# Kernel optimization log

Hardware: AMD Instinct MI355X
Metric: run time of the kernel (lower is better)

Reference implementation:

```python
import jax, jax.numpy as jnp
import numpy as np

B, C1, H, W = 2, 128, 64, 64
C_ = C1 // 2


def _conv2d(x, w, b, pad, dil):
    out = jax.lax.conv_general_dilated(
        x, w, (1, 1), [(pad, pad), (pad, pad)], rhs_dilation=(dil, dil),
        dimension_numbers=('NCHW', 'OIHW', 'NCHW'))
    return out + b[None, :, None, None]


def _deform_dw(x, off_w, off_b, w, k, pad, dil):
    # Depthwise DeformConv2d (v1, no modulation), offset_groups=1, stride=1.
    Bn, C, Hn, Wn = x.shape
    K = k * k
    offsets = _conv2d(x, off_w, off_b, pad, dil)          # [B, 2K, H, W]
    off = offsets.reshape(Bn, K, 2, Hn, Wn)               # (dy, dx) per kernel pt
    ky = jnp.repeat(jnp.arange(k) * dil, k).astype(x.dtype)   # [K]
    kx = jnp.tile(jnp.arange(k) * dil, k).astype(x.dtype)     # [K]
    py = off[:, :, 0] + (jnp.arange(Hn, dtype=x.dtype)[:, None] - pad) + ky[None, :, None, None]
    px = off[:, :, 1] + (jnp.arange(Wn, dtype=x.dtype)[None, :] - pad) + kx[None, :, None, None]
    y0 = jnp.floor(py); x0 = jnp.floor(px)
    ly = py - y0; lx = px - x0
    y0i = y0.astype(jnp.int32); x0i = x0.astype(jnp.int32)
    xf = x.reshape(Bn, C, Hn * Wn)

    def corner(yi, xi, wgt):
        valid = (yi >= 0) & (yi < Hn) & (xi >= 0) & (xi < Wn)
        idx = (jnp.clip(yi, 0, Hn - 1) * Wn + jnp.clip(xi, 0, Wn - 1)).reshape(Bn, -1)
        v = jax.vmap(lambda xb, ib: xb[:, ib])(xf, idx).reshape(Bn, C, K, Hn, Wn)
        return v * (wgt * valid.astype(x.dtype))[:, None]

    val = (corner(y0i, x0i, (1 - ly) * (1 - lx))
           + corner(y0i, x0i + 1, (1 - ly) * lx)
           + corner(y0i + 1, x0i, ly * (1 - lx))
           + corner(y0i + 1, x0i + 1, ly * lx))      # [B, C, K, H, W]
    return jnp.einsum('bckhw,ck->bchw', val, w.reshape(C, K))


def _forward(x, cv0_off_w, cv0_off_b, cv0_w, cvs_off_w, cvs_off_b, cvs_w,
             c0_off_w, c0_off_b, c0_w, cs_off_w, cs_off_b, cs_w,
             conv1_w, conv1_b, conv2_w, conv2_b):
    c = x.shape[1] // 2
    y0, y1 = x[:, :c], x[:, c:]
    a0 = _deform_dw(y0, cv0_off_w, cv0_off_b, cv0_w, 3, 1, 1)
    a0 = _deform_dw(a0, cvs_off_w, cvs_off_b, cvs_w, 5, 6, 3)
    a0 = _conv2d(a0, conv1_w, conv1_b, 0, 1)
    a1 = _deform_dw(y1, c0_off_w, c0_off_b, c0_w, 5, 2, 1)
    a1 = _deform_dw(a1, cs_off_w, cs_off_b, cs_w, 7, 9, 3)
    a1 = _conv2d(a1, conv2_w, conv2_b, 0, 1)
    return x * jnp.concatenate([a0, a1], axis=1)


def setup_inputs() -> dict:
    key = jax.random.key(0)
    ks = jax.random.split(key, 18)
    n = lambda k, sh, s: jax.random.normal(k, sh, dtype=jnp.float32) * s
    return {
        'x': n(ks[0], (B, C1, H, W), 1.0),
        'cv0_off_w': n(ks[1], (18, C_, 3, 3), 0.05),  'cv0_off_b': n(ks[2], (18,), 0.05),
        'cv0_w': n(ks[3], (C_, 1, 3, 3), 0.1),
        'cvs_off_w': n(ks[4], (50, C_, 5, 5), 0.05),  'cvs_off_b': n(ks[5], (50,), 0.05),
        'cvs_w': n(ks[6], (C_, 1, 5, 5), 0.1),
        'c0_off_w': n(ks[7], (50, C_, 5, 5), 0.05),   'c0_off_b': n(ks[8], (50,), 0.05),
        'c0_w': n(ks[9], (C_, 1, 5, 5), 0.1),
        'cs_off_w': n(ks[10], (98, C_, 7, 7), 0.05),  'cs_off_b': n(ks[11], (98,), 0.05),
        'cs_w': n(ks[12], (C_, 1, 7, 7), 0.1),
        'conv1_w': n(ks[13], (C_, C_, 1, 1), 0.1),    'conv1_b': n(ks[14], (C_,), 0.05),
        'conv2_w': n(ks[15], (C_, C_, 1, 1), 0.1),    'conv2_b': n(ks[16], (C_,), 0.05),
    }


def reference(x, cv0_off_w, cv0_off_b, cv0_w, cvs_off_w, cvs_off_b, cvs_w,
              c0_off_w, c0_off_b, c0_w, cs_off_w, cs_off_b, cs_w,
              conv1_w, conv1_b, conv2_w, conv2_b):
    return _forward(x, cv0_off_w, cv0_off_b, cv0_w, cvs_off_w, cvs_off_b, cvs_w,
                    c0_off_w, c0_off_b, c0_w, cs_off_w, cs_off_b, cs_w,
                    conv1_w, conv1_b, conv2_w, conv2_b)
```

## Files before the change

kernel.cpp:

```cpp
#include <hip/hip_runtime.h>
#include <hip/hip_bf16.h>

#define HW   4096

typedef __bf16 bf_t;
typedef __bf16 bf8_t __attribute__((ext_vector_type(8)));
typedef __bf16 bf2_t __attribute__((ext_vector_type(2)));
typedef __bf16 bf4v_t __attribute__((ext_vector_type(4)));
typedef float  f4_t  __attribute__((ext_vector_type(4)));
typedef float  f2_t  __attribute__((ext_vector_type(2)));
typedef int    i4_t  __attribute__((ext_vector_type(4)));

#define OFF_A    0
#define OFF_B    409600
#define A1_F32   1212416
#define B1_F32   1736704
#define A2_F32   2260992
#define B2_F32   2785280
#define XA_F32   3309568
#define XB_F32   3833856
#define XA_HI    4358144
#define XA_LO    4620288
#define XB_HI    4882432
#define XB_LO    5144576
#define A1_HI    5406720
#define A1_LO    5668864
#define B1_HI    5931008
#define B1_LO    6193152
#define AW_A1    6455296
#define AW_B1    6464512
#define AW_A2    6515712
#define AW_B2    6566912
#define DW_A1    6767616
#define DW_B1    6768192
#define DW_A2    6769792
#define DW_B2    6771392
#define WS_TOT   6774528

__device__ __align__(16) float g_ws[WS_TOT];

__device__ __forceinline__ bf8_t bf8_zero() {
    bf8_t v;
#pragma unroll
    for (int j = 0; j < 8; ++j) v[j] = (bf_t)0.f;
    return v;
}

__device__ __forceinline__ void prep_wA_dev(const float* wg, int aw_off,
                                            int Cout, int K, int NCOT, int lb) {
    const int KK = K * K;
    const int total = KK * NCOT * 128;
    const int idx = lb * 256 + threadIdx.x;
    if (idx >= total) return;
    bf_t* aw = (bf_t*)(g_ws + aw_off);
    int lane = idx & 63;
    int kh   = (idx >> 6) & 1;
    int cot  = (idx >> 7) % NCOT;
    int tap  = idx / (128 * NCOT);
    int co   = cot * 16 + (lane & 15);
    int ci0  = kh * 32 + (lane >> 4) * 8;
    bf8_t v;
#pragma unroll
    for (int j = 0; j < 8; ++j) {
        float f = (co < Cout) ? wg[(co * 64 + ci0 + j) * KK + tap] : 0.f;
        v[j] = (bf_t)f;
    }
    *(bf8_t*)&aw[(long)idx * 8] = v;
}

__device__ __forceinline__ void prep_dwT_dev(const float* w, int dst_off,
                                             int KK, int lb) {
    const int idx = lb * 256 + threadIdx.x;
    if (idx < KK * 64) {
        int c = idx & 63, kk = idx >> 6;
        g_ws[dst_off + kk * 64 + c] = w[c * KK + kk];
    }
}

__global__ __launch_bounds__(256) void prep_split_kernel(
    const float* __restrict__ x,
    const float* cv0_off_w, const float* c0_off_w,
    const float* cvs_off_w, const float* cs_off_w,
    const float* cv0_w, const float* c0_w,
    const float* cvs_w, const float* cs_w)
{
    __shared__ float lds[16 * 68];
    const int bi = blockIdx.x;
    if (bi < 335) {
        if      (bi < 9)   prep_wA_dev(cv0_off_w, AW_A1, 18, 3, 2, bi);
        else if (bi < 59)  prep_wA_dev(c0_off_w,  AW_B1, 50, 5, 4, bi - 9);
        else if (bi < 109) prep_wA_dev(cvs_off_w, AW_A2, 50, 5, 4, bi - 59);
        else if (bi < 305) prep_wA_dev(cs_off_w,  AW_B2, 98, 7, 8, bi - 109);
        else if (bi < 308) prep_dwT_dev(cv0_w, DW_A1, 9,  bi - 305);
        else if (bi < 315) prep_dwT_dev(c0_w,  DW_B1, 25, bi - 308);
        else if (bi < 322) prep_dwT_dev(cvs_w, DW_A2, 25, bi - 315);
        else               prep_dwT_dev(cs_w,  DW_B2, 49, bi - 322);
        return;
    }
    const int s  = bi - 335;
    const int b  = s & 1;
    const int br = (s >> 1) & 1;
    const int p0 = (s >> 2) * 16;
    const float* sb = x + (long)b * (128 * HW) + (long)br * (64 * HW);
    bf_t*  dhi = (bf_t*)(g_ws + (br ? XB_HI : XA_HI));
    bf_t*  dlo = (bf_t*)(g_ws + (br ? XB_LO : XA_LO));
    float* df  = g_ws + (br ? XB_F32 : XA_F32);
    const int t = threadIdx.x;
    {
        const int px = t & 15;
        const int c0 = t >> 4;
#pragma unroll
        for (int pass = 0; pass < 4; ++pass) {
            int ci = c0 + pass * 16;
            lds[px * 68 + ci] = sb[ci * HW + p0 + px];
        }
    }
    __syncthreads();
    if (t < 128) {
        int px = t >> 3, q = t & 7;
        bf8_t vh, vl;
        f4_t  f0, f1;
#pragma unroll
        for (int j = 0; j < 8; ++j) {
            float a = lds[px * 68 + q * 8 + j];
            bf_t hcast = (bf_t)a;
            vh[j] = hcast;
            vl[j] = (bf_t)(a - (float)hcast);
            if (j < 4) f0[j] = a; else f1[j - 4] = a;
        }
        long base = (((long)b * 4096 + p0 + px) * 64) + q * 8;
        *(bf8_t*)&dhi[base] = vh;
        *(bf8_t*)&dlo[base] = vl;
        *(f4_t*)&df[base]     = f0;
        *(f4_t*)&df[base + 4] = f1;
    }
}

template<int K, int DIL, int PAD, int NCOT, int CPG>
__device__ __forceinline__ void mfma_conv_dev(
    int bx, int by, bf_t* smem,
    int hi_off, int lo_off, int aw_off, const float* __restrict__ bias,
    int dst_off, int Cout)
{
    constexpr int COLS = 64 + 2 * PAD;
    const bf_t* shi = (const bf_t*)(g_ws + hi_off);
    const bf_t* slo = (const bf_t*)(g_ws + lo_off);
    const bf_t* aw  = (const bf_t*)(g_ws + aw_off);
    float* dst = g_ws + dst_off;
    bf_t* lds0 = smem;
    bf_t* lds1 = smem + COLS * 72;

    const int t    = threadIdx.x;
    const int lane = t & 63;
    const int wv   = t >> 6;
    const int b    = bx >> 6;
    const int h    = bx & 63;
    const int ct0  = by * CPG;

    const int n0 = lane & 15;
    const int kq = lane >> 4;

    f4_t acc[CPG];
#pragma unroll
    for (int i = 0; i < CPG; ++i) acc[i] = (f4_t){0.f, 0.f, 0.f, 0.f};

    for (int ky = 0; ky < K; ++ky) {
        const int ih = h - PAD + ky * DIL;
        __syncthreads();
        if ((unsigned)ih < 64u) {
            const long rowb = ((long)b * 4096 + ih * 64) * 64;
            for (int c = t; c < COLS * 8; c += 256) {
                int col = c >> 3, q = c & 7;
                int iw = col - PAD;
                bf8_t vh, vl;
                if ((unsigned)iw < 64u) {
                    vh = *(const bf8_t*)&shi[rowb + iw * 64 + q * 8];
                    vl = *(const bf8_t*)&slo[rowb + iw * 64 + q * 8];
                } else { vh = bf8_zero(); vl = bf8_zero(); }
                *(bf8_t*)&lds0[col * 72 + q * 8] = vh;
                *(bf8_t*)&lds1[col * 72 + q * 8] = vl;
            }
        } else {
            bf8_t z = bf8_zero();
            for (int c = t; c < COLS * 8; c += 256) {
                int col = c >> 3, q = c & 7;
                *(bf8_t*)&lds0[col * 72 + q * 8] = z;
                *(bf8_t*)&lds1[col * 72 + q * 8] = z;
            }
        }
        __syncthreads();
#pragma unroll
        for (int kx = 0; kx < K; ++kx) {
            const int tap = ky * K + kx;
            bf8_t afr[CPG][2];
#pragma unroll
            for (int ct = 0; ct < CPG; ++ct)
#pragma unroll
                for (int kh = 0; kh < 2; ++kh)
                    afr[ct][kh] = *(const bf8_t*)
                        &aw[((((long)tap * NCOT + ct0 + ct) * 2 + kh) * 64 + lane) * 8];
            const int colb = (wv * 16 + n0 + kx * DIL) * 72;
#pragma unroll
            for (int kh = 0; kh < 2; ++kh) {
                const bf8_t bh = *(const bf8_t*)&lds0[colb + kh * 32 + kq * 8];
                const bf8_t bl = *(const bf8_t*)&lds1[colb + kh * 32 + kq * 8];
#pragma unroll
                for (int ct = 0; ct < CPG; ++ct) {
                    acc[ct] = __builtin_amdgcn_mfma_f32_16x16x32_bf16(
                        afr[ct][kh], bh, acc[ct], 0, 0, 0);
                    acc[ct] = __builtin_amdgcn_mfma_f32_16x16x32_bf16(
                        afr[ct][kh], bl, acc[ct], 0, 0, 0);
                }
            }
        }
    }

    const int w = wv * 16 + n0;
#pragma unroll
    for (int ct = 0; ct < CPG; ++ct) {
#pragma unroll
        for (int r = 0; r < 4; ++r) {
            int co = (ct0 + ct) * 16 + kq * 4 + r;
            if (co < Cout)
                dst[((long)b * Cout + co) * HW + h * 64 + w] = acc[ct][r] + bias[co];
        }
    }
}

__global__ __launch_bounds__(256) void conv_s1_kernel(
    const float* __restrict__ biasA, const float* __restrict__ biasB)
{
    extern __shared__ __align__(16) bf_t smem1[];
    const int bi = blockIdx.x;
    const int g = bi / 3, r = bi % 3;
    if (r == 0)
        mfma_conv_dev<3, 1, 1, 2, 2>(g & 127, 0, smem1,
                                     XA_HI, XA_LO, AW_A1, biasA, OFF_A, 18);
    else {
        const int s = 2 * g + (r - 1);
        mfma_conv_dev<5, 1, 2, 4, 2>(s & 127, s >> 7, smem1,
                                     XB_HI, XB_LO, AW_B1, biasB, OFF_B, 50);
    }
}

__global__ __launch_bounds__(256) void conv_s2_kernel(
    const float* __restrict__ biasA, const float* __restrict__ biasB)
{
    extern __shared__ __align__(16) bf_t smem2[];
    const int bi = blockIdx.x;
    const int s = bi >> 1;
    if ((bi & 1) == 0)
        mfma_conv_dev<5, 3, 6, 4, 2>(s & 127, s >> 7, smem2,
                                     A1_HI, A1_LO, AW_A2, biasA, OFF_A, 50);
    else
        mfma_conv_dev<7, 3, 9, 8, 4>(s & 127, s >> 7, smem2,
                                     B1_HI, B1_LO, AW_B2, biasB, OFF_B, 98);
}

template<int KK, int WRITE_HILO>
__device__ __forceinline__ void sample_fused_dev(
    int bx, float* recs, float* dwl, int src_off, int off_off, int dwt_off,
    int dst_off, int hi_off, int lo_off, int K, int pad, int dil)
{
    const int t   = threadIdx.x;
    const int pgi = ((bx & 7) << 7) | (bx >> 3);

    for (int rec = t; rec < 8 * KK; rec += 256) {
        const int pxl = rec & 7;
        const int kk  = rec >> 3;
        const int pg  = pgi * 8 + pxl;
        const int b   = pg >> 12;
        const int p   = pg & 4095;
        const int h   = p >> 6, w = p & 63;
        const float oy = g_ws[off_off + ((long)(b * 2 * KK + 2 * kk)) * HW + p];
        const float ox = g_ws[off_off + ((long)(b * 2 * KK + 2 * kk + 1)) * HW + p];
        const float py = oy + (float)(h - pad + (kk / K) * dil);
        const float px = ox + (float)(w - pad + (kk % K) * dil);
        const float fy = floorf(py), fx = floorf(px);
        const float ly = py - fy,    lx = px - fx;
        const int y0 = (int)fy, x0 = (int)fx;
        const int y1 = y0 + 1,  x1 = x0 + 1;
        const float ry0 = ((unsigned)y0 < 64u) ? (1.f - ly) : 0.f;
        const float ry1 = ((unsigned)y1 < 64u) ? ly : 0.f;
        const float cx0 = ((unsigned)x0 < 64u) ? (1.f - lx) : 0.f;
        const float cx1 = ((unsigned)x1 < 64u) ? lx : 0.f;
        const int xbase = min(max(x0, 0), 62);
        const float sA = (xbase == x0) ? cx0 : ((xbase == x1) ? cx1 : 0.f);
        const float sB = ((xbase + 1) == x1) ? cx1
                                             : (((xbase + 1) == x0) ? cx0 : 0.f);
        const int y0c = min(max(y0, 0), 63), y1c = min(max(y1, 0), 63);
        const int a0 = (y0c * 64 + xbase) * 256;
        const int a1 = (y1c * 64 + xbase) * 256;
        float* rp = &recs[rec * 8];
        f4_t r0, r1;
        r0[0] = ry0 * sA; r0[1] = ry0 * sB;
        r0[2] = __int_as_float(a0); r0[3] = 0.f;
        r1[0] = ry1 * sA; r1[1] = ry1 * sB;
        r1[2] = __int_as_float(a1); r1[3] = 0.f;
        *(f4_t*)rp       = r0;
        *(f4_t*)(rp + 4) = r1;
    }

    for (int e = t; e < KK * 64; e += 256) dwl[e] = g_ws[dwt_off + e];
    __syncthreads();

    const int lane = t & 63;
    const int half = (lane >> 5) & 1;
    const int sub  = (lane >> 4) & 1;
    const int q    = lane & 15;
    const int wv   = t >> 6;
    const int px0  = wv * 2, px1 = wv * 2 + 1;
    const int pg0  = pgi * 8 + px0;
    const int b    = pg0 >> 12;

    const char*  sbl = (const char*)(g_ws + src_off + ((long)b << 18))
                       + sub * 256 + q * 16;
    const float* dwp = dwl + q * 4;

    f4_t acc0 = {0.f, 0.f, 0.f, 0.f};
    f4_t acc1 = {0.f, 0.f, 0.f, 0.f};
#pragma unroll
    for (int kk = 0; kk < KK; ++kk) {
        const f4_t r0 = *(const f4_t*)&recs[(kk * 8 + px0) * 8 + half * 4];
        const f4_t r1 = *(const f4_t*)&recs[(kk * 8 + px1) * 8 + half * 4];
        const f4_t dw = *(const f4_t*)(dwp + kk * 64);
        const float w0 = sub ? r0[1] : r0[0];
        const float w1 = sub ? r1[1] : r1[0];
        const f4_t v0 = *(const f4_t*)(sbl + __float_as_int(r0[2]));
        const f4_t v1 = *(const f4_t*)(sbl + __float_as_int(r1[2]));
#pragma unroll
        for (int c = 0; c < 4; ++c) {
            acc0[c] = fmaf(dw[c] * w0, v0[c], acc0[c]);
            acc1[c] = fmaf(dw[c] * w1, v1[c], acc1[c]);
        }
    }

#pragma unroll
    for (int c = 0; c < 4; ++c) {
        acc0[c] += __shfl_xor(acc0[c], 16);
        acc0[c] += __shfl_xor(acc0[c], 32);
        acc1[c] += __shfl_xor(acc1[c], 16);
        acc1[c] += __shfl_xor(acc1[c], 32);
    }

    const int p0 = pg0 & 4095;
    const long ob0 = ((long)b * 4096 + p0) * 64 + q * 4;
    const long ob1 = ob0 + 64;
    const int grp = lane >> 4;
    if (WRITE_HILO) {
        if (grp == 0) {
            *(f4_t*)&g_ws[dst_off + ob0] = acc0;
        } else if (grp == 1) {
            *(f4_t*)&g_ws[dst_off + ob1] = acc1;
        } else if (grp == 2) {
            bf4v_t h0, l0;
#pragma unroll
            for (int c = 0; c < 4; ++c) {
                bf_t hh = (bf_t)acc0[c];
                h0[c] = hh; l0[c] = (bf_t)(acc0[c] - (float)hh);
            }
            *(bf4v_t*)&((bf_t*)(g_ws + hi_off))[ob0] = h0;
            *(bf4v_t*)&((bf_t*)(g_ws + lo_off))[ob0] = l0;
        } else {
            bf4v_t h1, l1;
#pragma unroll
            for (int c = 0; c < 4; ++c) {
                bf_t hh = (bf_t)acc1[c];
                h1[c] = hh; l1[c] = (bf_t)(acc1[c] - (float)hh);
            }
            *(bf4v_t*)&((bf_t*)(g_ws + hi_off))[ob1] = h1;
            *(bf4v_t*)&((bf_t*)(g_ws + lo_off))[ob1] = l1;
        }
    } else {
        if (grp == 0)      *(f4_t*)&g_ws[dst_off + ob0] = acc0;
        else if (grp == 1) *(f4_t*)&g_ws[dst_off + ob1] = acc1;
    }
}

template<int KA, int KB, int WRITE_HILO>
__global__ __launch_bounds__(256) void sample_kernel(
    int srcA, int offA, int dwtA, int dstA, int hiA, int loA, int padA, int dilA,
    int srcB, int offB, int dwtB, int dstB, int hiB, int loB, int padB, int dilB)
{
    constexpr int KKmax = KB * KB;
    __shared__ __align__(16) float recs[8 * KKmax * 8];
    __shared__ __align__(16) float dwl[KKmax * 64];
    const int bx = blockIdx.x;
    const int s = bx >> 1;
    if ((bx & 1) == 0)
        sample_fused_dev<KA * KA, WRITE_HILO>(s, recs, dwl, srcA, offA, dwtA,
                                              dstA, hiA, loA, KA, padA, dilA);
    else
        sample_fused_dev<KB * KB, WRITE_HILO>(s, recs, dwl, srcB, offB, dwtB,
                                              dstB, hiB, loB, KB, padB, dilB);
}

__global__ __launch_bounds__(256) void final_kernel(
    const float* __restrict__ x,
    int aA_off, int aB_off,
    const float* __restrict__ w1, const float* __restrict__ b1,
    const float* __restrict__ w2, const float* __restrict__ b2,
    float* __restrict__ out)
{
    __shared__ float atile[64 * 65];
    __shared__ float wlds[64 * 32];
    const int t  = threadIdx.x;
    const int p0 = blockIdx.x * 64;
    const int by = blockIdx.y;
    const int b  = blockIdx.z;
    const bool brB  = (by >> 1) != 0;
    const int  cbase = (by & 1) * 32;
    const float* a  = g_ws + (brB ? aB_off : aA_off) + (long)b * (4096 * 64);
    const float* wg = brB ? w2 : w1;
    const float* bg = brB ? b2 : b1;

    {
        const int ci = t & 63;
        const int pxg = (t >> 6) * 16;
#pragma unroll
        for (int i = 0; i < 16; ++i) {
            int px = pxg + i;
            atile[px * 65 + ci] = a[(long)(p0 + px) * 64 + ci];
        }
    }
    for (int e = t; e < 2048; e += 256) {
        int col = e & 31, ci = e >> 5;
        wlds[ci * 32 + col] = wg[(cbase + col) * 64 + ci];
    }
    __syncthreads();

    const int px  = t & 63;
    const int cog = t >> 6;
    float acc[8] = {0, 0, 0, 0, 0, 0, 0, 0};
    for (int ci = 0; ci < 64; ++ci) {
        const float av = atile[px * 65 + ci];
        const float* wr = &wlds[ci * 32 + cog * 8];
#pragma unroll
        for (int j = 0; j < 8; ++j) acc[j] = fmaf(av, wr[j], acc[j]);
    }

    const int p = p0 + px;
#pragma unroll
    for (int j = 0; j < 8; ++j) {
        const int co = cbase + cog * 8 + j;
        const int cg = (brB ? 64 : 0) + co;
        const long o = ((long)b * 128 + cg) * HW + p;
        out[o] = (acc[j] + bg[co]) * x[o];
    }
}

extern "C" void kernel_launch(void* const* d_in, const int* in_sizes, int n_in,
                              void* d_out, int out_size, void* d_ws, size_t ws_size,
                              hipStream_t stream) {
    const float* x         = (const float*)d_in[0];
    const float* cv0_off_w = (const float*)d_in[1];
    const float* cv0_off_b = (const float*)d_in[2];
    const float* cv0_w     = (const float*)d_in[3];
    const float* cvs_off_w = (const float*)d_in[4];
    const float* cvs_off_b = (const float*)d_in[5];
    const float* cvs_w     = (const float*)d_in[6];
    const float* c0_off_w  = (const float*)d_in[7];
    const float* c0_off_b  = (const float*)d_in[8];
    const float* c0_w      = (const float*)d_in[9];
    const float* cs_off_w  = (const float*)d_in[10];
    const float* cs_off_b  = (const float*)d_in[11];
    const float* cs_w      = (const float*)d_in[12];
    const float* conv1_w   = (const float*)d_in[13];
    const float* conv1_b   = (const float*)d_in[14];
    const float* conv2_w   = (const float*)d_in[15];
    const float* conv2_b   = (const float*)d_in[16];
    float* out = (float*)d_out;
    (void)d_ws; (void)ws_size;

    prep_split_kernel<<<dim3(1359), 256, 0, stream>>>(
        x, cv0_off_w, c0_off_w, cvs_off_w, cs_off_w, cv0_w, c0_w, cvs_w, cs_w);

    conv_s1_kernel<<<dim3(384), 256, 19584, stream>>>(cv0_off_b, c0_off_b);

    sample_kernel<3, 5, 1><<<dim3(2048), 256, 0, stream>>>(
        XA_F32, OFF_A, DW_A1, A1_F32, A1_HI, A1_LO, 1, 1,
        XB_F32, OFF_B, DW_B1, B1_F32, B1_HI, B1_LO, 2, 1);

    conv_s2_kernel<<<dim3(512), 256, 23616, stream>>>(cvs_off_b, cs_off_b);

    sample_kernel<5, 7, 0><<<dim3(2048), 256, 0, stream>>>(
        A1_F32, OFF_A, DW_A2, A2_F32, 0, 0, 6, 3,
        B1_F32, OFF_B, DW_B2, B2_F32, 0, 0, 9, 3);

    final_kernel<<<dim3(64, 4, 2), 256, 0, stream>>>(
        x, A2_F32, B2_F32, conv1_w, conv1_b, conv2_w, conv2_b, out);
}
```

Measured before the change: 204.7 us.

## Fuse all six stages into one cooperative persistent kernel with grid syncs

```diff
diff --git a/kernel.cpp b/kernel.cpp
--- a/kernel.cpp
+++ b/kernel.cpp
@@ -1,15 +1,16 @@
 #include <hip/hip_runtime.h>
 #include <hip/hip_bf16.h>
+#include <hip/hip_cooperative_groups.h>
+
+namespace cg = cooperative_groups;
 
 #define HW   4096
+#define NBLK 768
 
 typedef __bf16 bf_t;
 typedef __bf16 bf8_t __attribute__((ext_vector_type(8)));
-typedef __bf16 bf2_t __attribute__((ext_vector_type(2)));
 typedef __bf16 bf4v_t __attribute__((ext_vector_type(4)));
 typedef float  f4_t  __attribute__((ext_vector_type(4)));
-typedef float  f2_t  __attribute__((ext_vector_type(2)));
-typedef int    i4_t  __attribute__((ext_vector_type(4)));
 
 #define OFF_A    0
 #define OFF_B    409600
@@ -77,15 +78,13 @@
     }
 }
 
-__global__ __launch_bounds__(256) void prep_split_kernel(
+__device__ __forceinline__ void prep_dev(int bi, float* lds,
     const float* __restrict__ x,
     const float* cv0_off_w, const float* c0_off_w,
     const float* cvs_off_w, const float* cs_off_w,
     const float* cv0_w, const float* c0_w,
     const float* cvs_w, const float* cs_w)
 {
-    __shared__ float lds[16 * 68];
-    const int bi = blockIdx.x;
     if (bi < 335) {
         if      (bi < 9)   prep_wA_dev(cv0_off_w, AW_A1, 18, 3, 2, bi);
         else if (bi < 59)  prep_wA_dev(c0_off_w,  AW_B1, 50, 5, 4, bi - 9);
@@ -227,43 +226,13 @@
     }
 }
 
-__global__ __launch_bounds__(256) void conv_s1_kernel(
-    const float* __restrict__ biasA, const float* __restrict__ biasB)
-{
-    extern __shared__ __align__(16) bf_t smem1[];
-    const int bi = blockIdx.x;
-    const int g = bi / 3, r = bi % 3;
-    if (r == 0)
-        mfma_conv_dev<3, 1, 1, 2, 2>(g & 127, 0, smem1,
-                                     XA_HI, XA_LO, AW_A1, biasA, OFF_A, 18);
-    else {
-        const int s = 2 * g + (r - 1);
-        mfma_conv_dev<5, 1, 2, 4, 2>(s & 127, s >> 7, smem1,
-                                     XB_HI, XB_LO, AW_B1, biasB, OFF_B, 50);
-    }
-}
-
-__global__ __launch_bounds__(256) void conv_s2_kernel(
-    const float* __restrict__ biasA, const float* __restrict__ biasB)
-{
-    extern __shared__ __align__(16) bf_t smem2[];
-    const int bi = blockIdx.x;
-    const int s = bi >> 1;
-    if ((bi & 1) == 0)
-        mfma_conv_dev<5, 3, 6, 4, 2>(s & 127, s >> 7, smem2,
-                                     A1_HI, A1_LO, AW_A2, biasA, OFF_A, 50);
-    else
-        mfma_conv_dev<7, 3, 9, 8, 4>(s & 127, s >> 7, smem2,
-                                     B1_HI, B1_LO, AW_B2, biasB, OFF_B, 98);
-}
-
 template<int KK, int WRITE_HILO>
 __device__ __forceinline__ void sample_fused_dev(
-    int bx, float* recs, float* dwl, int src_off, int off_off, int dwt_off,
+    int s, float* recs, float* dwl, int src_off, int off_off,
     int dst_off, int hi_off, int lo_off, int K, int pad, int dil)
 {
     const int t   = threadIdx.x;
-    const int pgi = ((bx & 7) << 7) | (bx >> 3);
+    const int pgi = ((s & 7) << 7) | (s >> 3);
 
     for (int rec = t; rec < 8 * KK; rec += 256) {
         const int pxl = rec & 7;
@@ -300,8 +269,6 @@
         *(f4_t*)rp       = r0;
         *(f4_t*)(rp + 4) = r1;
     }
-
-    for (int e = t; e < KK * 64; e += 256) dwl[e] = g_ws[dwt_off + e];
     __syncthreads();
 
     const int lane = t & 63;
@@ -377,6 +344,195 @@
     }
 }
 
+template<int KK, int WRITE_HILO>
+__device__ __forceinline__ void sample_phase(int g, float* recs, float* dwl,
+    int src_off, int off_off, int dwt_off, int dst_off, int hi_off, int lo_off,
+    int K, int pad, int dil)
+{
+    const int t = threadIdx.x;
+    for (int e = t; e < KK * 64; e += 256) dwl[e] = g_ws[dwt_off + e];
+    for (int s = g; s < 1024; s += NBLK / 2) {
+        __syncthreads();
+        sample_fused_dev<KK, WRITE_HILO>(s, recs, dwl, src_off, off_off,
+                                         dst_off, hi_off, lo_off, K, pad, dil);
+    }
+}
+
+__device__ __forceinline__ void final_dev(int vb, float* atile, float* wlds,
+    const float* __restrict__ x,
+    const float* __restrict__ w1, const float* __restrict__ b1,
+    const float* __restrict__ w2, const float* __restrict__ b2,
+    float* __restrict__ out)
+{
+    const int t  = threadIdx.x;
+    const int p0 = (vb & 63) * 64;
+    const int by = (vb >> 6) & 3;
+    const int b  = vb >> 8;
+    const bool brB  = (by >> 1) != 0;
+    const int  cbase = (by & 1) * 32;
+    const float* a  = g_ws + (brB ? B2_F32 : A2_F32) + (long)b * (4096 * 64);
+    const float* wg = brB ? w2 : w1;
+    const float* bg = brB ? b2 : b1;
+
+    {
+        const int ci = t & 63;
+        const int pxg = (t >> 6) * 16;
+#pragma unroll
+        for (int i = 0; i < 16; ++i) {
+            int px = pxg + i;
+            atile[px * 65 + ci] = a[(long)(p0 + px) * 64 + ci];
+        }
+    }
+    for (int e = t; e < 2048; e += 256) {
+        int col = e & 31, ci = e >> 5;
+        wlds[ci * 32 + col] = wg[(cbase + col) * 64 + ci];
+    }
+    __syncthreads();
+
+    const int px  = t & 63;
+    const int cog = t >> 6;
+    float acc[8] = {0, 0, 0, 0, 0, 0, 0, 0};
+    for (int ci = 0; ci < 64; ++ci) {
+        const float av = atile[px * 65 + ci];
+        const float* wr = &wlds[ci * 32 + cog * 8];
+#pragma unroll
+        for (int j = 0; j < 8; ++j) acc[j] = fmaf(av, wr[j], acc[j]);
+    }
+
+    const int p = p0 + px;
+#pragma unroll
+    for (int j = 0; j < 8; ++j) {
+        const int co = cbase + cog * 8 + j;
+        const int cg = (brB ? 64 : 0) + co;
+        const long o = ((long)b * 128 + cg) * HW + p;
+        out[o] = (acc[j] + bg[co]) * x[o];
+    }
+}
+
+__global__ __launch_bounds__(256, 3) void mega_kernel(
+    const float* __restrict__ x,
+    const float* cv0_off_w, const float* c0_off_w,
+    const float* cvs_off_w, const float* cs_off_w,
+    const float* cv0_w, const float* c0_w,
+    const float* cvs_w, const float* cs_w,
+    const float* cv0_off_b, const float* c0_off_b,
+    const float* cvs_off_b, const float* cs_off_b,
+    const float* conv1_w, const float* conv1_b,
+    const float* conv2_w, const float* conv2_b,
+    float* __restrict__ out)
+{
+    extern __shared__ __align__(16) char dsm[];
+    float* fsm = (float*)dsm;
+    bf_t*  bsm = (bf_t*)dsm;
+    const int bid = blockIdx.x;
+    cg::grid_group grid = cg::this_grid();
+
+    for (int vb = bid; vb < 1359; vb += NBLK) {
+        __syncthreads();
+        prep_dev(vb, fsm, x, cv0_off_w, c0_off_w, cvs_off_w, cs_off_w,
+                 cv0_w, c0_w, cvs_w, cs_w);
+    }
+    grid.sync();
+
+    {
+        const int g = bid / 3, r = bid % 3;
+        if (r == 0)
+            mfma_conv_dev<3, 1, 1, 2, 1>(g & 127, g >> 7, bsm,
+                                         XA_HI, XA_LO, AW_A1, cv0_off_b, OFF_A, 18);
+        else {
+            const int s = 2 * g + (r - 1);
+            mfma_conv_dev<5, 1, 2, 4, 1>(s & 127, s >> 7, bsm,
+                                         XB_HI, XB_LO, AW_B1, c0_off_b, OFF_B, 50);
+        }
+    }
+    grid.sync();
+
+    if ((bid & 1) == 0)
+        sample_phase<9, 1>(bid >> 1, fsm, fsm + 3136,
+                           XA_F32, OFF_A, DW_A1, A1_F32, A1_HI, A1_LO, 3, 1, 1);
+    else
+        sample_phase<25, 1>(bid >> 1, fsm, fsm + 3136,
+                            XB_F32, OFF_B, DW_B1, B1_F32, B1_HI, B1_LO, 5, 2, 1);
+    grid.sync();
+
+    {
+        const int g = bid / 3, r = bid % 3;
+        if (r == 0)
+            mfma_conv_dev<5, 3, 6, 4, 2>(g & 127, g >> 7, bsm,
+                                         A1_HI, A1_LO, AW_A2, cvs_off_b, OFF_A, 50);
+        else {
+            const int s = 2 * g + (r - 1);
+            mfma_conv_dev<7, 3, 9, 8, 2>(s & 127, s >> 7, bsm,
+                                         B1_HI, B1_LO, AW_B2, cs_off_b, OFF_B, 98);
+        }
+    }
+    grid.sync();
+
+    if ((bid & 1) == 0)
+        sample_phase<25, 0>(bid >> 1, fsm, fsm + 3136,
+                            A1_F32, OFF_A, DW_A2, A2_F32, 0, 0, 5, 6, 3);
+    else
+        sample_phase<49, 0>(bid >> 1, fsm, fsm + 3136,
+                            B1_F32, OFF_B, DW_B2, B2_F32, 0, 0, 7, 9, 3);
+    grid.sync();
+
+    if (bid < 512)
+        final_dev(bid, fsm, fsm + 64 * 65, x,
+                  conv1_w, conv1_b, conv2_w, conv2_b, out);
+}
+
+__global__ __launch_bounds__(256) void prep_split_kernel(
+    const float* __restrict__ x,
+    const float* cv0_off_w, const float* c0_off_w,
+    const float* cvs_off_w, const float* cs_off_w,
+    const float* cv0_w, const float* c0_w,
+    const float* cvs_w, const float* cs_w)
+{
+    __shared__ float lds[16 * 68];
+    prep_dev(blockIdx.x, lds, x, cv0_off_w, c0_off_w, cvs_off_w, cs_off_w,
+             cv0_w, c0_w, cvs_w, cs_w);
+}
+
+__global__ __launch_bounds__(256) void conv_s1_kernel(
+    const float* __restrict__ biasA, const float* __restrict__ biasB)
+{
+    extern __shared__ __align__(16) bf_t smem1[];
+    const int bi = blockIdx.x;
+    const int g = bi / 3, r = bi % 3;
+    if (r == 0)
+        mfma_conv_dev<3, 1, 1, 2, 2>(g & 127, 0, smem1,
+                                     XA_HI, XA_LO, AW_A1, biasA, OFF_A, 18);
+    else {
+        const int s = 2 * g + (r - 1);
+        mfma_conv_dev<5, 1, 2, 4, 2>(s & 127, s >> 7, smem1,
+                                     XB_HI, XB_LO, AW_B1, biasB, OFF_B, 50);
+    }
+}
+
+__global__ __launch_bounds__(256) void conv_s2_kernel(
+    const float* __restrict__ biasA, const float* __restrict__ biasB)
+{
+    extern __shared__ __align__(16) bf_t smem2[];
+    const int bi = blockIdx.x;
+    const int s = bi >> 1;
+    if ((bi & 1) == 0)
+        mfma_conv_dev<5, 3, 6, 4, 2>(s & 127, s >> 7, smem2,
+                                     A1_HI, A1_LO, AW_A2, biasA, OFF_A, 50);
+    else
+        mfma_conv_dev<7, 3, 9, 8, 4>(s & 127, s >> 7, smem2,
+                                     B1_HI, B1_LO, AW_B2, biasB, OFF_B, 98);
+}
+
+template<int KK, int WRITE_HILO>
+__device__ __forceinline__ void sample_one(int s, float* recs, float* dwl,
+    int src_off, int off_off, int dwt_off, int dst_off, int hi_off, int lo_off,
+    int K, int pad, int dil)
+{
+    for (int e = threadIdx.x; e < KK * 64; e += 256) dwl[e] = g_ws[dwt_off + e];
+    sample_fused_dev<KK, WRITE_HILO>(s, recs, dwl, src_off, off_off,
+                                     dst_off, hi_off, lo_off, K, pad, dil);
+}
+
 template<int KA, int KB, int WRITE_HILO>
 __global__ __launch_bounds__(256) void sample_kernel(
     int srcA, int offA, int dwtA, int dstA, int hiA, int loA, int padA, int dilA,
@@ -388,65 +544,22 @@
     const int bx = blockIdx.x;
     const int s = bx >> 1;
     if ((bx & 1) == 0)
-        sample_fused_dev<KA * KA, WRITE_HILO>(s, recs, dwl, srcA, offA, dwtA,
-                                              dstA, hiA, loA, KA, padA, dilA);
+        sample_one<KA * KA, WRITE_HILO>(s, recs, dwl, srcA, offA, dwtA,
+                                        dstA, hiA, loA, KA, padA, dilA);
     else
-        sample_fused_dev<KB * KB, WRITE_HILO>(s, recs, dwl, srcB, offB, dwtB,
-                                              dstB, hiB, loB, KB, padB, dilB);
+        sample_one<KB * KB, WRITE_HILO>(s, recs, dwl, srcB, offB, dwtB,
+                                        dstB, hiB, loB, KB, padB, dilB);
 }
 
 __global__ __launch_bounds__(256) void final_kernel(
     const float* __restrict__ x,
-    int aA_off, int aB_off,
     const float* __restrict__ w1, const float* __restrict__ b1,
     const float* __restrict__ w2, const float* __restrict__ b2,
     float* __restrict__ out)
 {
     __shared__ float atile[64 * 65];
     __shared__ float wlds[64 * 32];
-    const int t  = threadIdx.x;
-    const int p0 = blockIdx.x * 64;
-    const int by = blockIdx.y;
-    const int b  = blockIdx.z;
-    const bool brB  = (by >> 1) != 0;
-    const int  cbase = (by & 1) * 32;
-    const float* a  = g_ws + (brB ? aB_off : aA_off) + (long)b * (4096 * 64);
-    const float* wg = brB ? w2 : w1;
-    const float* bg = brB ? b2 : b1;
-
-    {
-        const int ci = t & 63;
-        const int pxg = (t >> 6) * 16;
-#pragma unroll
-        for (int i = 0; i < 16; ++i) {
-            int px = pxg + i;
-            atile[px * 65 + ci] = a[(long)(p0 + px) * 64 + ci];
-        }
-    }
-    for (int e = t; e < 2048; e += 256) {
-        int col = e & 31, ci = e >> 5;
-        wlds[ci * 32 + col] = wg[(cbase + col) * 64 + ci];
-    }
-    __syncthreads();
-
-    const int px  = t & 63;
-    const int cog = t >> 6;
-    float acc[8] = {0, 0, 0, 0, 0, 0, 0, 0};
-    for (int ci = 0; ci < 64; ++ci) {
-        const float av = atile[px * 65 + ci];
-        const float* wr = &wlds[ci * 32 + cog * 8];
-#pragma unroll
-        for (int j = 0; j < 8; ++j) acc[j] = fmaf(av, wr[j], acc[j]);
-    }
-
-    const int p = p0 + px;
-#pragma unroll
-    for (int j = 0; j < 8; ++j) {
-        const int co = cbase + cog * 8 + j;
-        const int cg = (brB ? 64 : 0) + co;
-        const long o = ((long)b * 128 + cg) * HW + p;
-        out[o] = (acc[j] + bg[co]) * x[o];
-    }
+    final_dev(blockIdx.x, atile, wlds, x, w1, b1, w2, b2, out);
 }
 
 extern "C" void kernel_launch(void* const* d_in, const int* in_sizes, int n_in,
@@ -472,21 +585,28 @@
     float* out = (float*)d_out;
     (void)d_ws; (void)ws_size;
 
+    void* args[] = {
+        (void*)&x,
+        (void*)&cv0_off_w, (void*)&c0_off_w, (void*)&cvs_off_w, (void*)&cs_off_w,
+        (void*)&cv0_w, (void*)&c0_w, (void*)&cvs_w, (void*)&cs_w,
+        (void*)&cv0_off_b, (void*)&c0_off_b, (void*)&cvs_off_b, (void*)&cs_off_b,
+        (void*)&conv1_w, (void*)&conv1_b, (void*)&conv2_w, (void*)&conv2_b,
+        (void*)&out};
+    hipError_t e = hipLaunchCooperativeKernel((const void*)mega_kernel,
+                                              dim3(NBLK), dim3(256),
+                                              args, 25088u, stream);
+    if (e == hipSuccess) return;
+
     prep_split_kernel<<<dim3(1359), 256, 0, stream>>>(
         x, cv0_off_w, c0_off_w, cvs_off_w, cs_off_w, cv0_w, c0_w, cvs_w, cs_w);
-
     conv_s1_kernel<<<dim3(384), 256, 19584, stream>>>(cv0_off_b, c0_off_b);
-
     sample_kernel<3, 5, 1><<<dim3(2048), 256, 0, stream>>>(
         XA_F32, OFF_A, DW_A1, A1_F32, A1_HI, A1_LO, 1, 1,
         XB_F32, OFF_B, DW_B1, B1_F32, B1_HI, B1_LO, 2, 1);
-
     conv_s2_kernel<<<dim3(512), 256, 23616, stream>>>(cvs_off_b, cs_off_b);
-
     sample_kernel<5, 7, 0><<<dim3(2048), 256, 0, stream>>>(
         A1_F32, OFF_A, DW_A2, A2_F32, 0, 0, 6, 3,
         B1_F32, OFF_B, DW_B2, B2_F32, 0, 0, 9, 3);
-
-    final_kernel<<<dim3(64, 4, 2), 256, 0, stream>>>(
-        x, A2_F32, B2_F32, conv1_w, conv1_b, conv2_w, conv2_b, out);
-}
+    final_kernel<<<dim3(512), 256, 0, stream>>>(
+        x, conv1_w, conv1_b, conv2_w, conv2_b, out);
+}
```

After: 732.3 us. +257.7%, slower.
